# Performance work log

Hardware: AMD Instinct MI355X
Metric: run time of the kernel (lower is better)

Reference implementation:

```python
import jax, jax.numpy as jnp
import numpy as np

C_S = 1024
C_Z = 128
H = 16
D = C_S // H  # 64
INF = 1000000.0
B, I, J = 1, 1024, 1024


def setup_inputs() -> dict:
    key = jax.random.key(0)
    ks = jax.random.split(key, 10)
    sc = 0.02
    return {
        "s": jax.random.normal(ks[0], (B, I, C_S), jnp.float32),
        "k_in": jax.random.normal(ks[1], (B, J, C_S), jnp.float32),
        "mask": jnp.ones((B, J), jnp.float32),
        "bias": jax.random.normal(ks[2], (B, I, J, C_Z), jnp.float32),
        "Wq": jax.random.normal(ks[3], (C_S, C_S), jnp.float32) * sc,
        "bq": jax.random.normal(ks[4], (C_S,), jnp.float32) * sc,
        "Wk": jax.random.normal(ks[5], (C_S, C_S), jnp.float32) * sc,
        "Wv": jax.random.normal(ks[6], (C_S, C_S), jnp.float32) * sc,
        "Wg": jax.random.normal(ks[7], (C_S, C_S), jnp.float32) * sc,
        "Wo": jax.random.normal(ks[8], (C_S, C_S), jnp.float32) * sc,
        "Wz": jax.random.normal(ks[9], (C_Z, H), jnp.float32) * sc,
        "multiplicity": 1,
    }


def reference(s, k_in, mask, bias, Wq, bq, Wk, Wv, Wg, Wo, Wz, multiplicity):
    b = s.shape[0]
    # QKV projections (torch Linear: x @ W.T + b)
    q = (s @ Wq.T + bq).reshape(b, -1, H, D)        # [b, i, h, d]
    k = (k_in @ Wk.T).reshape(b, -1, H, D)          # [b, j, h, d]
    v = (k_in @ Wv.T).reshape(b, -1, H, D)          # [b, j, h, d]

    # pair bias: proj_z = Linear(c_z -> h, no bias) + rearrange to [b, h, i, j]
    z = jnp.einsum("bijc,ch->bhij", bias, Wz)
    z = jnp.repeat(z, multiplicity, axis=0)
    z = z + (1.0 - mask[:, None, None, :]) * (-INF)  # mask over key dim j

    g = jax.nn.sigmoid(s @ Wg.T)                    # [b, i, c_s]

    # attention in fp32 (original uses autocast-disabled fp32 block)
    attn = jnp.einsum("bihd,bjhd->bhij", q.astype(jnp.float32), k.astype(jnp.float32))
    attn = attn / (D ** 0.5) + z.astype(jnp.float32)
    attn = jax.nn.softmax(attn, axis=-1)
    o = jnp.einsum("bhij,bjhd->bihd", attn, v.astype(jnp.float32)).astype(v.dtype)

    o = o.reshape(b, -1, C_S)
    return (g * o) @ Wo.T
```

## Files before the change

kernel.cpp:

```cpp
#include <hip/hip_runtime.h>

typedef unsigned short u16;
typedef unsigned int   u32;
typedef __attribute__((ext_vector_type(8))) short bf16x8;
typedef __attribute__((ext_vector_type(4))) float f32x4;

#define MFMA16(a, b, c) __builtin_amdgcn_mfma_f32_16x16x32_bf16((a), (b), (c), 0, 0, 0)

__device__ __forceinline__ float bfu(u16 x) { return __uint_as_float(((u32)x) << 16); }
__device__ __forceinline__ u16 f2bf(float f) {
    u32 u = __float_as_uint(f);
    u32 r = u + 0x7fffu + ((u >> 16) & 1u);
    return (u16)(r >> 16);
}
__device__ __forceinline__ u32 pk2(float a, float b) {
    return (u32)f2bf(a) | ((u32)f2bf(b) << 16);
}
__device__ __forceinline__ u32 bfmul2(u32 a, u32 b) {
    float lo = bfu((u16)(a & 0xffffu)) * bfu((u16)(b & 0xffffu));
    float hi = bfu((u16)(a >> 16))     * bfu((u16)(b >> 16));
    return pk2(lo, hi);
}
__device__ __forceinline__ bf16x8 cvt8(float4 a, float4 b) {
    bf16x8 r;
    r[0] = (short)f2bf(a.x); r[1] = (short)f2bf(a.y);
    r[2] = (short)f2bf(a.z); r[3] = (short)f2bf(a.w);
    r[4] = (short)f2bf(b.x); r[5] = (short)f2bf(b.y);
    r[6] = (short)f2bf(b.z); r[7] = (short)f2bf(b.w);
    return r;
}

struct CvtArgs { const float* src[7]; u16* dst[7]; };

__global__ __launch_bounds__(256) void convert_bf16(CvtArgs a) {
    const int tsel = blockIdx.x >> 6;
    const int blk  = blockIdx.x & 63;
    const float* s = a.src[tsel];
    u16* d = a.dst[tsel];
    const int base = blk * 16384;
    #pragma unroll 4
    for (int it = 0; it < 16; ++it) {
        const int idx = base + (it * 256 + threadIdx.x) * 4;
        float4 v = *(const float4*)(s + idx);
        uint2 p;
        p.x = pk2(v.x, v.y);
        p.y = pk2(v.z, v.w);
        *(uint2*)(d + idx) = p;
    }
}

template<int AMODE, int OMODE, bool BIASF, bool SIGF>
__global__ __launch_bounds__(256) void gemm64(
    const u16* __restrict__ Ab, const u16* __restrict__ Gb,
    const u16* __restrict__ W, const float* __restrict__ biasv,
    void* __restrict__ Cp)
{
    __shared__ u16 lA[64 * 40];
    __shared__ u16 lB[64 * 40];
    const int t = threadIdx.x;
    const int lane = t & 63, w = t >> 6;
    const int ln = lane & 15, q4 = lane >> 4;
    const int wm = (w & 1) * 32, wn = (w >> 1) * 32;
    const int m0 = blockIdx.y * 64, n0 = blockIdx.x * 64;
    const int lrow = t >> 2, lk = (t & 3) * 8;

    f32x4 acc00 = {0,0,0,0}, acc01 = {0,0,0,0}, acc10 = {0,0,0,0}, acc11 = {0,0,0,0};

    for (int k0 = 0; k0 < 1024; k0 += 32) {
        const int idx = (m0 + lrow) * 1024 + k0 + lk;
        uint4 ra = *(const uint4*)(Ab + idx);
        if (AMODE == 1) {
            uint4 rg = *(const uint4*)(Gb + idx);
            ra.x = bfmul2(ra.x, rg.x);
            ra.y = bfmul2(ra.y, rg.y);
            ra.z = bfmul2(ra.z, rg.z);
            ra.w = bfmul2(ra.w, rg.w);
        }
        uint4 rb = *(const uint4*)(W + (n0 + lrow) * 1024 + k0 + lk);
        *(uint4*)(lA + lrow * 40 + lk) = ra;
        *(uint4*)(lB + lrow * 40 + lk) = rb;
        __syncthreads();

        bf16x8 af0 = *(const bf16x8*)(lA + (wm +      ln) * 40 + q4 * 8);
        bf16x8 af1 = *(const bf16x8*)(lA + (wm + 16 + ln) * 40 + q4 * 8);
        bf16x8 bf0 = *(const bf16x8*)(lB + (wn +      ln) * 40 + q4 * 8);
        bf16x8 bf1 = *(const bf16x8*)(lB + (wn + 16 + ln) * 40 + q4 * 8);
        acc00 = MFMA16(af0, bf0, acc00);
        acc01 = MFMA16(af0, bf1, acc01);
        acc10 = MFMA16(af1, bf0, acc10);
        acc11 = MFMA16(af1, bf1, acc11);
        __syncthreads();
    }

    #pragma unroll
    for (int tm = 0; tm < 2; ++tm) {
        #pragma unroll
        for (int tn = 0; tn < 2; ++tn) {
            const f32x4 a = (tm == 0) ? (tn == 0 ? acc00 : acc01)
                                      : (tn == 0 ? acc10 : acc11);
            #pragma unroll
            for (int r = 0; r < 4; ++r) {
                const int gm = m0 + wm + tm * 16 + q4 * 4 + r;
                const int gn = n0 + wn + tn * 16 + ln;
                float cv = a[r];
                if (BIASF) cv += biasv[gn];
                if (SIGF)  cv = 1.0f / (1.0f + __expf(-cv));
                if (OMODE == 0)      ((float*)Cp)[gm * 1024 + gn] = cv;
                else if (OMODE == 1) ((u16*)Cp)[gm * 1024 + gn] = f2bf(cv);
                else                 ((u16*)Cp)[gn * 1024 + gm] = f2bf(cv);
            }
        }
    }
}

__global__ __launch_bounds__(256) void zproj(
    const float* __restrict__ bias, const float* __restrict__ Wz, u16* __restrict__ z)
{
    __shared__ float lz[16 * 516];
    const int t = threadIdx.x, lane = t & 63, w = t >> 6;
    const int ln = lane & 15, q4 = lane >> 4;
    const int row0 = blockIdx.x * 512;

    bf16x8 bfrag[4];
    #pragma unroll
    for (int kb = 0; kb < 4; ++kb)
        #pragma unroll
        for (int j = 0; j < 8; ++j)
            bfrag[kb][j] = (short)f2bf(Wz[(kb * 32 + q4 * 8 + j) * 16 + ln]);

    #pragma unroll 1
    for (int it = 0; it < 8; ++it) {
        const int rloc = (it * 4 + w) * 16;
        const float* ap = bias + (size_t)(row0 + rloc + ln) * 128 + q4 * 8;
        f32x4 c = {0, 0, 0, 0};
        #pragma unroll
        for (int kb = 0; kb < 4; ++kb) {
            float4 x0 = *(const float4*)(ap + kb * 32);
            float4 x1 = *(const float4*)(ap + kb * 32 + 4);
            bf16x8 a = cvt8(x0, x1);
            c = MFMA16(a, bfrag[kb], c);
        }
        #pragma unroll
        for (int r = 0; r < 4; ++r)
            lz[ln * 516 + rloc + q4 * 4 + r] = c[r];
    }
    __syncthreads();
    #pragma unroll 4
    for (int rep = 0; rep < 32; ++rep) {
        const int idx = rep * 256 + t;
        const int hh = idx >> 9, r = idx & 511;
        z[(size_t)hh * 1048576 + row0 + r] = f2bf(lz[hh * 516 + r]);
    }
}

__global__ __launch_bounds__(256) void attn_kernel(
    const u16* __restrict__ qb, const u16* __restrict__ kb,
    const u16* __restrict__ vT, const u16* __restrict__ zb,
    const float* __restrict__ maskb, u16* __restrict__ o)
{
    __shared__ u16 pbf[16 * 1032];
    __shared__ float redm[4][16];
    __shared__ float reds[4][16];
    const int h = blockIdx.y;
    const int i0 = blockIdx.x * 16;
    const int t = threadIdx.x, lane = t & 63, w = t >> 6;
    const int ln = lane & 15, q4 = lane >> 4;

    const u16* qp = qb + (i0 + ln) * 1024 + h * 64 + q4 * 8;
    const bf16x8 aq0 = *(const bf16x8*)(qp);
    const bf16x8 aq1 = *(const bf16x8*)(qp + 32);

    f32x4 s[16];
    #pragma unroll
    for (int u = 0; u < 16; ++u) {
        const int j0 = (w * 16 + u) * 16;
        const u16* kp = kb + (j0 + ln) * 1024 + h * 64 + q4 * 8;
        bf16x8 b0 = *(const bf16x8*)(kp);
        bf16x8 b1 = *(const bf16x8*)(kp + 32);
        f32x4 c = {0, 0, 0, 0};
        c = MFMA16(aq0, b0, c);
        c = MFMA16(aq1, b1, c);
        const int j = j0 + ln;
        const float mt = (1.0f - maskb[j]) * (-1000000.0f);
        #pragma unroll
        for (int r = 0; r < 4; ++r) {
            const int gi = i0 + q4 * 4 + r;
            c[r] = c[r] * 0.125f + bfu(zb[(size_t)h * 1048576 + gi * 1024 + j]) + mt;
        }
        s[u] = c;
    }

    float mx[4];
    #pragma unroll
    for (int r = 0; r < 4; ++r) {
        float m_ = s[0][r];
        #pragma unroll
        for (int u = 1; u < 16; ++u) m_ = fmaxf(m_, s[u][r]);
        #pragma unroll
        for (int off = 1; off < 16; off <<= 1) m_ = fmaxf(m_, __shfl_xor(m_, off));
        mx[r] = m_;
    }
    if (ln == 0) {
        #pragma unroll
        for (int r = 0; r < 4; ++r) redm[w][q4 * 4 + r] = mx[r];
    }
    __syncthreads();

    float inv[4];
    #pragma unroll
    for (int r = 0; r < 4; ++r) {
        const int row = q4 * 4 + r;
        const float m_ = fmaxf(fmaxf(redm[0][row], redm[1][row]),
                               fmaxf(redm[2][row], redm[3][row]));
        float s_ = 0.f;
        #pragma unroll
        for (int u = 0; u < 16; ++u) {
            float e = __expf(s[u][r] - m_);
            s[u][r] = e;
            s_ += e;
        }
        #pragma unroll
        for (int off = 1; off < 16; off <<= 1) s_ += __shfl_xor(s_, off);
        mx[r] = s_;
    }
    if (ln == 0) {
        #pragma unroll
        for (int r = 0; r < 4; ++r) reds[w][q4 * 4 + r] = mx[r];
    }
    __syncthreads();
    #pragma unroll
    for (int r = 0; r < 4; ++r) {
        const int row = q4 * 4 + r;
        inv[r] = 1.0f / (reds[0][row] + reds[1][row] + reds[2][row] + reds[3][row]);
    }

    #pragma unroll
    for (int u = 0; u < 16; ++u) {
        const int j0 = (w * 16 + u) * 16;
        #pragma unroll
        for (int r = 0; r < 4; ++r)
            pbf[(q4 * 4 + r) * 1032 + j0 + ln] = f2bf(s[u][r] * inv[r]);
    }
    __syncthreads();

    f32x4 oc = {0, 0, 0, 0};
    #pragma unroll 4
    for (int ks = 0; ks < 32; ++ks) {
        bf16x8 pa = *(const bf16x8*)(pbf + ln * 1032 + ks * 32 + q4 * 8);
        bf16x8 vb = *(const bf16x8*)(vT + (h * 64 + w * 16 + ln) * 1024 + ks * 32 + q4 * 8);
        oc = MFMA16(pa, vb, oc);
    }
    #pragma unroll
    for (int r = 0; r < 4; ++r)
        o[(i0 + q4 * 4 + r) * 1024 + h * 64 + w * 16 + ln] = f2bf(oc[r]);
}

extern "C" void kernel_launch(void* const* d_in, const int* in_sizes, int n_in,
                              void* d_out, int out_size, void* d_ws, size_t ws_size,
                              hipStream_t stream)
{
    const float* s_in = (const float*)d_in[0];
    const float* k_in = (const float*)d_in[1];
    const float* mask = (const float*)d_in[2];
    const float* bias = (const float*)d_in[3];
    const float* Wq   = (const float*)d_in[4];
    const float* bq   = (const float*)d_in[5];
    const float* Wk   = (const float*)d_in[6];
    const float* Wv   = (const float*)d_in[7];
    const float* Wg   = (const float*)d_in[8];
    const float* Wo   = (const float*)d_in[9];
    const float* Wz   = (const float*)d_in[10];

    char* ws = (char*)d_ws;
    const size_t MB = 1 << 20;
    u16* sb  = (u16*)(ws + 0 * MB);
    u16* kbf = (u16*)(ws + 2 * MB);
    u16* Wqb = (u16*)(ws + 4 * MB);
    u16* Wkb = (u16*)(ws + 6 * MB);
    u16* Wvb = (u16*)(ws + 8 * MB);
    u16* Wgb = (u16*)(ws + 10 * MB);
    u16* Wob = (u16*)(ws + 12 * MB);
    u16* q   = (u16*)(ws + 14 * MB);
    u16* kk  = (u16*)(ws + 16 * MB);
    u16* vT  = (u16*)(ws + 18 * MB);
    u16* g   = (u16*)(ws + 20 * MB);
    u16* o   = (u16*)(ws + 22 * MB);
    u16* z   = (u16*)(ws + 24 * MB);
    float* out = (float*)d_out;

    CvtArgs ca;
    ca.src[0] = s_in; ca.dst[0] = sb;
    ca.src[1] = k_in; ca.dst[1] = kbf;
    ca.src[2] = Wq;   ca.dst[2] = Wqb;
    ca.src[3] = Wk;   ca.dst[3] = Wkb;
    ca.src[4] = Wv;   ca.dst[4] = Wvb;
    ca.src[5] = Wg;   ca.dst[5] = Wgb;
    ca.src[6] = Wo;   ca.dst[6] = Wob;

    const dim3 gg(16, 16), blk(256);
    hipLaunchKernelGGL(convert_bf16, dim3(448), blk, 0, stream, ca);
    hipLaunchKernelGGL((gemm64<0, 1, true,  false>), gg, blk, 0, stream, sb,  nullptr, Wqb, bq,      q);
    hipLaunchKernelGGL((gemm64<0, 1, false, false>), gg, blk, 0, stream, kbf, nullptr, Wkb, nullptr, kk);
    hipLaunchKernelGGL((gemm64<0, 2, false, false>), gg, blk, 0, stream, kbf, nullptr, Wvb, nullptr, vT);
    hipLaunchKernelGGL((gemm64<0, 1, false, true >), gg, blk, 0, stream, sb,  nullptr, Wgb, nullptr, g);
    hipLaunchKernelGGL(zproj, dim3(2048), blk, 0, stream, bias, Wz, z);
    hipLaunchKernelGGL(attn_kernel, dim3(64, 16), blk, 0, stream, q, kk, vT, z, mask, o);
    hipLaunchKernelGGL((gemm64<1, 0, false, false>), gg, blk, 0, stream, o, g, Wob, nullptr, out);
}
```

Baseline: 845.3 us.

## Merge projection GEMMs, use direct global-to-LDS loads, fuse gate into attention

Rewrites the GEMM to load tiles with global_load_lds and use a 64-wide K step. The Q/G and K/V projections now run as two wider launches instead of four. The sigmoid gate multiply moves from the output GEMM's A-load into the attention epilogue. This cuts launch count, per-k-step barrier overhead and the per-element bf16 multiply in the Wo GEMM. The risk is LDS bank conflicts, since the unpadded 64-stride layout replaces the padded 40 stride.

```diff
diff --git a/kernel.cpp b/kernel.cpp
--- a/kernel.cpp
+++ b/kernel.cpp
@@ -15,11 +15,6 @@
 }
 __device__ __forceinline__ u32 pk2(float a, float b) {
     return (u32)f2bf(a) | ((u32)f2bf(b) << 16);
-}
-__device__ __forceinline__ u32 bfmul2(u32 a, u32 b) {
-    float lo = bfu((u16)(a & 0xffffu)) * bfu((u16)(b & 0xffffu));
-    float hi = bfu((u16)(a >> 16))     * bfu((u16)(b >> 16));
-    return pk2(lo, hi);
 }
 __device__ __forceinline__ bf16x8 cvt8(float4 a, float4 b) {
     bf16x8 r;
@@ -28,6 +23,11 @@
     r[4] = (short)f2bf(b.x); r[5] = (short)f2bf(b.y);
     r[6] = (short)f2bf(b.z); r[7] = (short)f2bf(b.w);
     return r;
+}
+__device__ __forceinline__ void gl_lds16(const u16* g, u16* l) {
+    __builtin_amdgcn_global_load_lds(
+        (const __attribute__((address_space(1))) void*)g,
+        (__attribute__((address_space(3))) void*)l, 16, 0, 0);
 }
 
 struct CvtArgs { const float* src[7]; u16* dst[7]; };
@@ -49,46 +49,45 @@
     }
 }
 
-template<int AMODE, int OMODE, bool BIASF, bool SIGF>
-__global__ __launch_bounds__(256) void gemm64(
-    const u16* __restrict__ Ab, const u16* __restrict__ Gb,
-    const u16* __restrict__ W, const float* __restrict__ biasv,
-    void* __restrict__ Cp)
+template<int EPI>
+__global__ __launch_bounds__(256) void gemmW(
+    const u16* __restrict__ Ab, const u16* __restrict__ W0, const u16* __restrict__ W1,
+    const float* __restrict__ bqv, void* __restrict__ C0, void* __restrict__ C1)
 {
-    __shared__ u16 lA[64 * 40];
-    __shared__ u16 lB[64 * 40];
-    const int t = threadIdx.x;
-    const int lane = t & 63, w = t >> 6;
+    __shared__ u16 lA[64 * 64];
+    __shared__ u16 lB[64 * 64];
+    const int t = threadIdx.x, lane = t & 63, w = t >> 6;
     const int ln = lane & 15, q4 = lane >> 4;
     const int wm = (w & 1) * 32, wn = (w >> 1) * 32;
     const int m0 = blockIdx.y * 64, n0 = blockIdx.x * 64;
-    const int lrow = t >> 2, lk = (t & 3) * 8;
+
+    const u16* Wp = (n0 < 1024) ? (W0 + (size_t)n0 * 1024)
+                                : (W1 + (size_t)(n0 - 1024) * 1024);
+    const int srow = t >> 3, scol = (t & 7) * 8;
+    const u16* ga = Ab + (m0 + srow) * 1024 + scol;
+    const u16* gb = Wp + srow * 1024 + scol;
+    u16* la = lA + t * 8;
+    u16* lb = lB + t * 8;
 
     f32x4 acc00 = {0,0,0,0}, acc01 = {0,0,0,0}, acc10 = {0,0,0,0}, acc11 = {0,0,0,0};
 
-    for (int k0 = 0; k0 < 1024; k0 += 32) {
-        const int idx = (m0 + lrow) * 1024 + k0 + lk;
-        uint4 ra = *(const uint4*)(Ab + idx);
-        if (AMODE == 1) {
-            uint4 rg = *(const uint4*)(Gb + idx);
-            ra.x = bfmul2(ra.x, rg.x);
-            ra.y = bfmul2(ra.y, rg.y);
-            ra.z = bfmul2(ra.z, rg.z);
-            ra.w = bfmul2(ra.w, rg.w);
-        }
-        uint4 rb = *(const uint4*)(W + (n0 + lrow) * 1024 + k0 + lk);
-        *(uint4*)(lA + lrow * 40 + lk) = ra;
-        *(uint4*)(lB + lrow * 40 + lk) = rb;
+    for (int k0 = 0; k0 < 1024; k0 += 64) {
+        gl_lds16(ga + k0,             la);
+        gl_lds16(ga + k0 + 32 * 1024, la + 32 * 64);
+        gl_lds16(gb + k0,             lb);
+        gl_lds16(gb + k0 + 32 * 1024, lb + 32 * 64);
         __syncthreads();
-
-        bf16x8 af0 = *(const bf16x8*)(lA + (wm +      ln) * 40 + q4 * 8);
-        bf16x8 af1 = *(const bf16x8*)(lA + (wm + 16 + ln) * 40 + q4 * 8);
-        bf16x8 bf0 = *(const bf16x8*)(lB + (wn +      ln) * 40 + q4 * 8);
-        bf16x8 bf1 = *(const bf16x8*)(lB + (wn + 16 + ln) * 40 + q4 * 8);
-        acc00 = MFMA16(af0, bf0, acc00);
-        acc01 = MFMA16(af0, bf1, acc01);
-        acc10 = MFMA16(af1, bf0, acc10);
-        acc11 = MFMA16(af1, bf1, acc11);
+        #pragma unroll
+        for (int ks = 0; ks < 2; ++ks) {
+            bf16x8 a0 = *(const bf16x8*)(lA + (wm +      ln) * 64 + ks * 32 + q4 * 8);
+            bf16x8 a1 = *(const bf16x8*)(lA + (wm + 16 + ln) * 64 + ks * 32 + q4 * 8);
+            bf16x8 b0 = *(const bf16x8*)(lB + (wn +      ln) * 64 + ks * 32 + q4 * 8);
+            bf16x8 b1 = *(const bf16x8*)(lB + (wn + 16 + ln) * 64 + ks * 32 + q4 * 8);
+            acc00 = MFMA16(a0, b0, acc00);
+            acc01 = MFMA16(a0, b1, acc01);
+            acc10 = MFMA16(a1, b0, acc10);
+            acc11 = MFMA16(a1, b1, acc11);
+        }
         __syncthreads();
     }
 
@@ -103,11 +102,16 @@
                 const int gm = m0 + wm + tm * 16 + q4 * 4 + r;
                 const int gn = n0 + wn + tn * 16 + ln;
                 float cv = a[r];
-                if (BIASF) cv += biasv[gn];
-                if (SIGF)  cv = 1.0f / (1.0f + __expf(-cv));
-                if (OMODE == 0)      ((float*)Cp)[gm * 1024 + gn] = cv;
-                else if (OMODE == 1) ((u16*)Cp)[gm * 1024 + gn] = f2bf(cv);
-                else                 ((u16*)Cp)[gn * 1024 + gm] = f2bf(cv);
+                if (EPI == 0) {
+                    if (gn < 1024) ((u16*)C0)[gm * 1024 + gn] = f2bf(cv + bqv[gn]);
+                    else ((u16*)C1)[gm * 1024 + gn - 1024] =
+                             f2bf(1.0f / (1.0f + __expf(-cv)));
+                } else if (EPI == 1) {
+                    if (gn < 1024) ((u16*)C0)[gm * 1024 + gn] = f2bf(cv);
+                    else ((u16*)C1)[(gn - 1024) * 1024 + gm] = f2bf(cv);
+                } else {
+                    ((float*)C0)[gm * 1024 + gn] = cv;
+                }
             }
         }
     }
@@ -154,9 +158,10 @@
 }
 
 __global__ __launch_bounds__(256) void attn_kernel(
-    const u16* __restrict__ qb, const u16* __restrict__ kb,
+    const u16* __restrict__ qb, const u16* __restrict__ kmat,
     const u16* __restrict__ vT, const u16* __restrict__ zb,
-    const float* __restrict__ maskb, u16* __restrict__ o)
+    const float* __restrict__ maskb, const u16* __restrict__ gmat,
+    u16* __restrict__ o)
 {
     __shared__ u16 pbf[16 * 1032];
     __shared__ float redm[4][16];
@@ -174,7 +179,7 @@
     #pragma unroll
     for (int u = 0; u < 16; ++u) {
         const int j0 = (w * 16 + u) * 16;
-        const u16* kp = kb + (j0 + ln) * 1024 + h * 64 + q4 * 8;
+        const u16* kp = kmat + (j0 + ln) * 1024 + h * 64 + q4 * 8;
         bf16x8 b0 = *(const bf16x8*)(kp);
         bf16x8 b1 = *(const bf16x8*)(kp + 32);
         f32x4 c = {0, 0, 0, 0};
@@ -250,9 +255,13 @@
         bf16x8 vb = *(const bf16x8*)(vT + (h * 64 + w * 16 + ln) * 1024 + ks * 32 + q4 * 8);
         oc = MFMA16(pa, vb, oc);
     }
-    #pragma unroll
-    for (int r = 0; r < 4; ++r)
-        o[(i0 + q4 * 4 + r) * 1024 + h * 64 + w * 16 + ln] = f2bf(oc[r]);
+    const int col = h * 64 + w * 16 + ln;
+    #pragma unroll
+    for (int r = 0; r < 4; ++r) {
+        const int gi = i0 + q4 * 4 + r;
+        const float gv = bfu(gmat[gi * 1024 + col]);
+        o[gi * 1024 + col] = f2bf(oc[r] * gv);
+    }
 }
 
 extern "C" void kernel_launch(void* const* d_in, const int* in_sizes, int n_in,
@@ -284,7 +293,7 @@
     u16* kk  = (u16*)(ws + 16 * MB);
     u16* vT  = (u16*)(ws + 18 * MB);
     u16* g   = (u16*)(ws + 20 * MB);
-    u16* o   = (u16*)(ws + 22 * MB);
+    u16* og  = (u16*)(ws + 22 * MB);
     u16* z   = (u16*)(ws + 24 * MB);
     float* out = (float*)d_out;
 
@@ -297,13 +306,11 @@
     ca.src[5] = Wg;   ca.dst[5] = Wgb;
     ca.src[6] = Wo;   ca.dst[6] = Wob;
 
-    const dim3 gg(16, 16), blk(256);
+    const dim3 blk(256);
     hipLaunchKernelGGL(convert_bf16, dim3(448), blk, 0, stream, ca);
-    hipLaunchKernelGGL((gemm64<0, 1, true,  false>), gg, blk, 0, stream, sb,  nullptr, Wqb, bq,      q);
-    hipLaunchKernelGGL((gemm64<0, 1, false, false>), gg, blk, 0, stream, kbf, nullptr, Wkb, nullptr, kk);
-    hipLaunchKernelGGL((gemm64<0, 2, false, false>), gg, blk, 0, stream, kbf, nullptr, Wvb, nullptr, vT);
-    hipLaunchKernelGGL((gemm64<0, 1, false, true >), gg, blk, 0, stream, sb,  nullptr, Wgb, nullptr, g);
+    hipLaunchKernelGGL(gemmW<0>, dim3(32, 16), blk, 0, stream, sb,  Wqb, Wgb, bq, q,  g);
+    hipLaunchKernelGGL(gemmW<1>, dim3(32, 16), blk, 0, stream, kbf, Wkb, Wvb, nullptr, kk, vT);
     hipLaunchKernelGGL(zproj, dim3(2048), blk, 0, stream, bias, Wz, z);
-    hipLaunchKernelGGL(attn_kernel, dim3(64, 16), blk, 0, stream, q, kk, vT, z, mask, o);
-    hipLaunchKernelGGL((gemm64<1, 0, false, false>), gg, blk, 0, stream, o, g, Wob, nullptr, out);
-}
+    hipLaunchKernelGGL(attn_kernel, dim3(64, 16), blk, 0, stream, q, kk, vT, z, mask, g, og);
+    hipLaunchKernelGGL(gemmW<2>, dim3(16, 16), blk, 0, stream, og, Wob, nullptr, nullptr, out, nullptr);
+}
```

Result: faster. 814.3 us (-3.7%).
